# Performance work log

Hardware: AMD Instinct MI355X
Metric: run time of the kernel (lower is better)

## Reference

```python
import jax, jax.numpy as jnp
import numpy as np
import math

B, S, D, H = 2, 4096, 512, 8
DK = D // H


def setup_inputs() -> dict:
    key = jax.random.key(0)
    ks = jax.random.split(key, 9)
    s = 1.0 / math.sqrt(D)
    return {
        "x": jax.random.normal(ks[0], (B, S, D), dtype=jnp.float32),
        "Wq": jax.random.normal(ks[1], (D, D), dtype=jnp.float32) * s,
        "bq": jax.random.normal(ks[2], (D,), dtype=jnp.float32) * 0.01,
        "Wk": jax.random.normal(ks[3], (D, D), dtype=jnp.float32) * s,
        "bk": jax.random.normal(ks[4], (D,), dtype=jnp.float32) * 0.01,
        "Wv": jax.random.normal(ks[5], (D, D), dtype=jnp.float32) * s,
        "bv": jax.random.normal(ks[6], (D,), dtype=jnp.float32) * 0.01,
        "Wo": jax.random.normal(ks[7], (D, D), dtype=jnp.float32) * s,
        "bo": jax.random.normal(ks[8], (D,), dtype=jnp.float32) * 0.01,
    }


def reference(x, Wq, bq, Wk, bk, Wv, bv, Wo, bo):
    b, s, _ = x.shape
    # projections, split into heads: (b, h, s, dk)
    def proj(W, bias):
        return (x @ W.T + bias).reshape(b, s, H, DK).transpose(0, 2, 1, 3)
    Q, K, V = proj(Wq, bq), proj(Wk, bk), proj(Wv, bv)
    scale = 1.0 / math.sqrt(DK)
    scores = jnp.einsum("bhqd,bhkd->bhqk", Q, K) * scale  # (b,h,s,s)
    causal = jnp.tril(jnp.ones((s, s), dtype=bool))
    scores = jnp.where(causal[None, None], scores, -jnp.inf)
    attn = jax.nn.softmax(scores, axis=-1)
    out = jnp.einsum("bhqk,bhkd->bhqd", attn, V)
    out = out.transpose(0, 2, 1, 3).reshape(b, s, D)
    return out @ Wo.T + bo
```

## Files before the change

kernel.cpp:

```cpp
#include <hip/hip_runtime.h>
#include <hip/hip_bf16.h>

using u16    = unsigned short;
using u32    = unsigned int;
using bf16x8 = __attribute__((ext_vector_type(8))) __bf16;
using s16x4  = __attribute__((ext_vector_type(4))) short;
using f32x4  = __attribute__((ext_vector_type(4))) float;
using u16x4  = __attribute__((ext_vector_type(4))) unsigned short;
using u16x8  = __attribute__((ext_vector_type(8))) unsigned short;
using u32x2  = __attribute__((ext_vector_type(2))) unsigned int;
using u32x4  = __attribute__((ext_vector_type(4))) unsigned int;


static __device__ __forceinline__ u16 f2bf(float f) {
  unsigned int u = __float_as_uint(f);
  u += 0x7fffu + ((u >> 16) & 1u);
  return (u16)(u >> 16);
}
static __device__ __forceinline__ u32 pack2bf(float lo, float hi) {
  return __builtin_amdgcn_perm(__float_as_uint(hi), __float_as_uint(lo), 0x07060302u);
}

__global__ __launch_bounds__(256) void cvt_all(
    const float* __restrict__ x,  const float* __restrict__ wq,
    const float* __restrict__ wk, const float* __restrict__ wv,
    const float* __restrict__ wo,
    u16* __restrict__ xb, u16* __restrict__ wqb, u16* __restrict__ wkb,
    u16* __restrict__ wvb, u16* __restrict__ wob) {
  const int bx = blockIdx.x;
  const float* src;
  u16* dst;
  int i;
  if (bx < 4096) {
    src = x; dst = xb; i = bx * 256 + threadIdx.x;
  } else {
    const int t  = (bx - 4096) >> 8;
    const int lb = (bx - 4096) & 255;
    src = (t == 0) ? wq : (t == 1) ? wk : (t == 2) ? wv : wo;
    dst = (t == 0) ? wqb : (t == 1) ? wkb : (t == 2) ? wvb : wob;
    i = lb * 256 + threadIdx.x;
  }
  float4 v = reinterpret_cast<const float4*>(src)[i];
  u16x4 o = { f2bf(v.x), f2bf(v.y), f2bf(v.z), f2bf(v.w) };
  reinterpret_cast<u16x4*>(dst)[i] = o;
}

__global__ __launch_bounds__(256, 3) void gemm_qkv(const u16* __restrict__ A,
                                                   const u16* __restrict__ Wq,
                                                   const u16* __restrict__ Wk,
                                                   const u16* __restrict__ Wv,
                                                   const float* __restrict__ bqp,
                                                   const float* __restrict__ bkp,
                                                   const float* __restrict__ bvp,
                                                   u16* __restrict__ Qo,
                                                   u16* __restrict__ Ko,
                                                   u16* __restrict__ Vto) {
  const int which = blockIdx.z;
  const u16* W = (which == 0) ? Wq : (which == 1) ? Wk : Wv;
  const float* bias = (which == 0) ? bqp : (which == 1) ? bkp : bvp;

  __shared__ u16 sA[128 * 72];
  __shared__ u16 sB[128 * 72];
  const int row0 = blockIdx.x * 128;
  const int col0 = blockIdx.y * 128;
  const int tid  = threadIdx.x;
  const int lane = tid & 63;
  const int wave = tid >> 6;
  const int wm   = (wave & 1) * 64;
  const int wn   = (wave >> 1) * 64;
  const int ln   = lane & 15;
  const int quad = lane >> 4;

  int rr[4], cc[4];
  for (int i = 0; i < 4; ++i) {
    const int idx = tid + 256 * i;
    rr[i] = idx >> 3; cc[i] = (idx & 7) * 8;
  }

  f32x4 zero = {0.f, 0.f, 0.f, 0.f};
  f32x4 acc[4][4];
  for (int i = 0; i < 4; ++i)
    for (int j = 0; j < 4; ++j) acc[i][j] = zero;

  u16x8 curA[4], nxtA[4];
  for (int i = 0; i < 4; ++i)
    curA[i] = *reinterpret_cast<const u16x8*>(&A[(row0 + rr[i]) * 512 + cc[i]]);

  for (int k0 = 0; k0 < 512; k0 += 64) {
    __syncthreads();
    for (int i = 0; i < 4; ++i) {
      *reinterpret_cast<u16x8*>(&sA[rr[i] * 72 + cc[i]]) = curA[i];
      *reinterpret_cast<u16x8*>(&sB[rr[i] * 72 + cc[i]]) =
          *reinterpret_cast<const u16x8*>(&W[(col0 + rr[i]) * 512 + k0 + cc[i]]);
    }
    if (k0 < 448)
      for (int i = 0; i < 4; ++i)
        nxtA[i] = *reinterpret_cast<const u16x8*>(&A[(row0 + rr[i]) * 512 + k0 + 64 + cc[i]]);
    __syncthreads();
    for (int ks = 0; ks < 2; ++ks) {
      bf16x8 af[4], bfr[4];
      for (int t4 = 0; t4 < 4; ++t4)
        af[t4] = *reinterpret_cast<const bf16x8*>(&sA[(wm + t4 * 16 + ln) * 72 + ks * 32 + quad * 8]);
      for (int t4 = 0; t4 < 4; ++t4)
        bfr[t4] = *reinterpret_cast<const bf16x8*>(&sB[(wn + t4 * 16 + ln) * 72 + ks * 32 + quad * 8]);
      for (int tm = 0; tm < 4; ++tm)
        for (int tn = 0; tn < 4; ++tn)
          acc[tm][tn] = __builtin_amdgcn_mfma_f32_16x16x32_bf16(af[tm], bfr[tn], acc[tm][tn], 0, 0, 0);
    }
    for (int i = 0; i < 4; ++i) curA[i] = nxtA[i];
  }

  if (which < 2) {
    u16* out = (which == 0) ? Qo : Ko;
    const float scale = (which == 0) ? 0.125f : 1.0f;
    for (int tm = 0; tm < 4; ++tm) {
      const int mbase = row0 + wm + tm * 16 + quad * 4;
      for (int tn = 0; tn < 4; ++tn) {
        const int n  = col0 + wn + tn * 16 + ln;
        const int h  = n >> 6, dk = n & 63;
        const float bv = bias[n];
        for (int r = 0; r < 4; ++r) {
          const int m  = mbase + r;
          const int bh = ((m >> 12) << 3) + h;
          const int s  = m & 4095;
          out[(bh * 4096 + s) * 64 + dk] = f2bf((acc[tm][tn][r] + bv) * scale);
        }
      }
    }
  } else {
    for (int tm = 0; tm < 4; ++tm) {
      const int mbase = row0 + wm + tm * 16 + quad * 4;
      const int b_idx = mbase >> 12;
      const int s     = mbase & 4095;
      for (int tn = 0; tn < 4; ++tn) {
        const int n  = col0 + wn + tn * 16 + ln;
        const int h  = n >> 6, dk = n & 63;
        const int bh = b_idx * 8 + h;
        const float bv = bias[n];
        u16x4 o;
        for (int r = 0; r < 4; ++r) o[r] = f2bf(acc[tm][tn][r] + bv);
        *reinterpret_cast<u16x4*>(&Vto[(bh * 64 + dk) * 4096 + s]) = o;
      }
    }
  }
}

__global__ __launch_bounds__(256, 3) void gemm_out(const u16* __restrict__ A,
                                                   const u16* __restrict__ W,
                                                   const float* __restrict__ bias,
                                                   float* __restrict__ out) {
  __shared__ u16 sA[128 * 72];
  __shared__ u16 sB[128 * 72];
  const int row0 = blockIdx.x * 128;
  const int col0 = blockIdx.y * 128;
  const int tid  = threadIdx.x;
  const int lane = tid & 63;
  const int wave = tid >> 6;
  const int wm   = (wave & 1) * 64;
  const int wn   = (wave >> 1) * 64;
  const int ln   = lane & 15;
  const int quad = lane >> 4;

  int rr[4], cc[4];
  for (int i = 0; i < 4; ++i) {
    const int idx = tid + 256 * i;
    rr[i] = idx >> 3; cc[i] = (idx & 7) * 8;
  }

  f32x4 zero = {0.f, 0.f, 0.f, 0.f};
  f32x4 acc[4][4];
  for (int i = 0; i < 4; ++i)
    for (int j = 0; j < 4; ++j) acc[i][j] = zero;

  u16x8 curA[4], nxtA[4];
  for (int i = 0; i < 4; ++i)
    curA[i] = *reinterpret_cast<const u16x8*>(&A[(row0 + rr[i]) * 512 + cc[i]]);

  for (int k0 = 0; k0 < 512; k0 += 64) {
    __syncthreads();
    for (int i = 0; i < 4; ++i) {
      *reinterpret_cast<u16x8*>(&sA[rr[i] * 72 + cc[i]]) = curA[i];
      *reinterpret_cast<u16x8*>(&sB[rr[i] * 72 + cc[i]]) =
          *reinterpret_cast<const u16x8*>(&W[(col0 + rr[i]) * 512 + k0 + cc[i]]);
    }
    if (k0 < 448)
      for (int i = 0; i < 4; ++i)
        nxtA[i] = *reinterpret_cast<const u16x8*>(&A[(row0 + rr[i]) * 512 + k0 + 64 + cc[i]]);
    __syncthreads();
    for (int ks = 0; ks < 2; ++ks) {
      bf16x8 af[4], bfr[4];
      for (int t4 = 0; t4 < 4; ++t4)
        af[t4] = *reinterpret_cast<const bf16x8*>(&sA[(wm + t4 * 16 + ln) * 72 + ks * 32 + quad * 8]);
      for (int t4 = 0; t4 < 4; ++t4)
        bfr[t4] = *reinterpret_cast<const bf16x8*>(&sB[(wn + t4 * 16 + ln) * 72 + ks * 32 + quad * 8]);
      for (int tm = 0; tm < 4; ++tm)
        for (int tn = 0; tn < 4; ++tn)
          acc[tm][tn] = __builtin_amdgcn_mfma_f32_16x16x32_bf16(af[tm], bfr[tn], acc[tm][tn], 0, 0, 0);
    }
    for (int i = 0; i < 4; ++i) curA[i] = nxtA[i];
  }

  for (int tm = 0; tm < 4; ++tm) {
    const int mbase = row0 + wm + tm * 16 + quad * 4;
    for (int tn = 0; tn < 4; ++tn) {
      const int n  = col0 + wn + tn * 16 + ln;
      const float bv = bias[n];
      for (int r = 0; r < 4; ++r)
        out[(mbase + r) * 512 + n] = acc[tm][tn][r] + bv;
    }
  }
}

#if __has_builtin(__builtin_amdgcn_mfma_f32_16x16x16bf16_1k)
#define HAVE_MFMA16 1
#endif
__global__ __launch_bounds__(256, 4) void attn_part(const u16* __restrict__ Q,
                                                    const u16* __restrict__ K,
                                                    const u16* __restrict__ Vt,
                                                    float* __restrict__ pO,
                                                    float* __restrict__ pl) {
  const int c = blockIdx.x;
  const int t = blockIdx.y;
  const int ga = t >> 3;
  if (c > ga) return;
  const int ktlast = 2 * t + 1;
  const int kt0 = 16 * c;
  const int kt1 = (kt0 + 15 < ktlast) ? (kt0 + 15) : ktlast;
  const int bh = blockIdx.z;
  const int qb = t * 128;

  const u16* Qh  = Q  + bh * 4096 * 64;
  const u16* Kh  = K  + bh * 4096 * 64;
  const u16* Vth = Vt + bh * 64 * 4096;

  __shared__ u16 sK[64 * 72];
  __shared__ u16 sV[64 * 72];

  const int tid  = threadIdx.x;
  const int lane = tid & 63;
  const int wave = tid >> 6;
  const int ln   = lane & 15;
  const int quad = lane >> 4;

  const int r0 = tid >> 3,         c0 = (tid & 7) * 8;
  const int r1 = (tid + 256) >> 3, c1 = ((tid + 256) & 7) * 8;

  bf16x8 qf[2][2];
  for (int tn = 0; tn < 2; ++tn)
    for (int ks = 0; ks < 2; ++ks)
      qf[tn][ks] = *reinterpret_cast<const bf16x8*>(
          &Qh[(qb + wave * 32 + tn * 16 + ln) * 64 + ks * 32 + quad * 8]);

  f32x4 zero = {0.f, 0.f, 0.f, 0.f};
  f32x4 accO[4][2];
  float lsum[2] = {0.f, 0.f};
  for (int td = 0; td < 4; ++td)
    for (int tn = 0; tn < 2; ++tn) accO[td][tn] = zero;

#ifndef HAVE_MFMA16
  const int idx0 = 4 * (ln + 16 * (2 * (quad & 1)));
#endif

  u16x8 cur[4], nxt[4];
  {
    const int kb = kt0 * 64;
    cur[0] = *reinterpret_cast<const u16x8*>(&Kh[(kb + r0) * 64 + c0]);
    cur[1] = *reinterpret_cast<const u16x8*>(&Kh[(kb + r1) * 64 + c1]);
    cur[2] = *reinterpret_cast<const u16x8*>(&Vth[r0 * 4096 + kb + c0]);
    cur[3] = *reinterpret_cast<const u16x8*>(&Vth[r1 * 4096 + kb + c1]);
  }

  for (int kt = kt0; kt <= kt1; ++kt) {
    const int kb = kt * 64;
    __syncthreads();
    *reinterpret_cast<u16x8*>(&sK[r0 * 72 + c0]) = cur[0];
    *reinterpret_cast<u16x8*>(&sK[r1 * 72 + c1]) = cur[1];
    *reinterpret_cast<u16x8*>(&sV[r0 * 72 + c0]) = cur[2];
    *reinterpret_cast<u16x8*>(&sV[r1 * 72 + c1]) = cur[3];
    if (kt < kt1) {
      const int kn = kb + 64;
      nxt[0] = *reinterpret_cast<const u16x8*>(&Kh[(kn + r0) * 64 + c0]);
      nxt[1] = *reinterpret_cast<const u16x8*>(&Kh[(kn + r1) * 64 + c1]);
      nxt[2] = *reinterpret_cast<const u16x8*>(&Vth[r0 * 4096 + kn + c0]);
      nxt[3] = *reinterpret_cast<const u16x8*>(&Vth[r1 * 4096 + kn + c1]);
    }
    __syncthreads();

    f32x4 accS[4][2];
    for (int tm = 0; tm < 4; ++tm)
      for (int tn = 0; tn < 2; ++tn) accS[tm][tn] = zero;
    for (int tm = 0; tm < 4; ++tm) {
      bf16x8 kf0 = *reinterpret_cast<const bf16x8*>(&sK[(tm * 16 + ln) * 72 + quad * 8]);
      bf16x8 kf1 = *reinterpret_cast<const bf16x8*>(&sK[(tm * 16 + ln) * 72 + 32 + quad * 8]);
      for (int tn = 0; tn < 2; ++tn) {
        accS[tm][tn] = __builtin_amdgcn_mfma_f32_16x16x32_bf16(kf0, qf[tn][0], accS[tm][tn], 0, 0, 0);
        accS[tm][tn] = __builtin_amdgcn_mfma_f32_16x16x32_bf16(kf1, qf[tn][1], accS[tm][tn], 0, 0, 0);
      }
    }

    const bool diag = (kt >= 2 * t);
    u32 pp[4][2][2];
    for (int tm = 0; tm < 4; ++tm)
      for (int tn = 0; tn < 2; ++tn) {
        f32x4 e = accS[tm][tn];
        if (diag) {
          const int kg = kb + tm * 16 + quad * 4;
          const int qg = qb + wave * 32 + tn * 16 + ln;
          for (int r = 0; r < 4; ++r)
            if (kg + r > qg) e[r] = -__builtin_inff();
        }
        for (int r = 0; r < 4; ++r) e[r] = __expf(e[r]);
        lsum[tn] += (e[0] + e[1]) + (e[2] + e[3]);
        pp[tm][tn][0] = pack2bf(e[0], e[1]);
        pp[tm][tn][1] = pack2bf(e[2], e[3]);
      }

#ifdef HAVE_MFMA16
    for (int k16 = 0; k16 < 4; ++k16)
      for (int td = 0; td < 4; ++td) {
        s16x4 vf = *reinterpret_cast<const s16x4*>(&sV[(td * 16 + ln) * 72 + k16 * 16 + quad * 4]);
        for (int tn = 0; tn < 2; ++tn) {
          u32x2 pr = { pp[k16][tn][0], pp[k16][tn][1] };
          s16x4 pb = __builtin_bit_cast(s16x4, pr);
          accO[td][tn] = __builtin_amdgcn_mfma_f32_16x16x16bf16_1k(vf, pb, accO[td][tn], 0, 0, 0);
        }
      }
#else
    for (int ks = 0; ks < 2; ++ks)
      for (int tn = 0; tn < 2; ++tn) {
        u32 b[4];
        for (int half = 0; half < 2; ++half)
          for (int p = 0; p < 2; ++p) {
            int v0 = __builtin_amdgcn_ds_bpermute(idx0 + 64 * half, (int)pp[2 * ks][tn][p]);
            int v1 = __builtin_amdgcn_ds_bpermute(idx0 + 64 * half, (int)pp[2 * ks + 1][tn][p]);
            b[half * 2 + p] = (quad < 2) ? (u32)v0 : (u32)v1;
          }
        u32x4 bv4 = { b[0], b[1], b[2], b[3] };
        bf16x8 pfrag = __builtin_bit_cast(bf16x8, bv4);
        for (int td = 0; td < 4; ++td) {
          bf16x8 vf = *reinterpret_cast<const bf16x8*>(&sV[(td * 16 + ln) * 72 + ks * 32 + quad * 8]);
          accO[td][tn] = __builtin_amdgcn_mfma_f32_16x16x32_bf16(vf, pfrag, accO[td][tn], 0, 0, 0);
        }
      }
#endif
    for (int j = 0; j < 4; ++j) cur[j] = nxt[j];
  }

  for (int tn = 0; tn < 2; ++tn) {
    lsum[tn] += __shfl_xor(lsum[tn], 16);
    lsum[tn] += __shfl_xor(lsum[tn], 32);
  }
  const int slot = bh * 80 + t + 4 * ga * (ga - 1) + ga * (t & 7) + c;
  float* po = pO + (size_t)slot * 8192;
  for (int td = 0; td < 4; ++td)
    for (int tn = 0; tn < 2; ++tn)
      for (int r = 0; r < 4; ++r)
        po[(td * 16 + quad * 4 + r) * 128 + wave * 32 + tn * 16 + ln] = accO[td][tn][r];
  if (quad == 0)
    for (int tn = 0; tn < 2; ++tn)
      pl[slot * 128 + wave * 32 + tn * 16 + ln] = lsum[tn];
}

__global__ __launch_bounds__(256) void attn_comb(const float* __restrict__ pO,
                                                 const float* __restrict__ pl,
                                                 u16* __restrict__ ctx) {
  const int t  = blockIdx.x;
  const int bh = blockIdx.y;
  const int ga = t >> 3;
  const int nch = ga + 1;
  const int base = bh * 80 + t + 4 * ga * (ga - 1) + ga * (t & 7);
  const int tid = threadIdx.x;

  __shared__ float sO[64 * 132];
  __shared__ float sL[128];

  float4 acc[8];
  for (int i = 0; i < 8; ++i) acc[i] = make_float4(0.f, 0.f, 0.f, 0.f);
  float lacc = 0.f;
  for (int cidx = 0; cidx < nch; ++cidx) {
    const float* src = pO + (size_t)(base + cidx) * 8192;
    for (int i = 0; i < 8; ++i) {
      float4 v = reinterpret_cast<const float4*>(src)[i * 256 + tid];
      acc[i].x += v.x; acc[i].y += v.y; acc[i].z += v.z; acc[i].w += v.w;
    }
    if (tid < 128) lacc += pl[(base + cidx) * 128 + tid];
  }
  for (int i = 0; i < 8; ++i) {
    const int f = i * 256 + tid;
    const int d = f >> 5, q = (f & 31) * 4;
    *reinterpret_cast<float4*>(&sO[d * 132 + q]) = acc[i];
  }
  if (tid < 128) sL[tid] = lacc;
  __syncthreads();

  const int q  = tid >> 1;
  const int d0 = (tid & 1) * 32;
  const float inv = 1.0f / sL[q];
  const int b_idx = bh >> 3, h = bh & 7;
  const int tok = (b_idx << 12) + t * 128 + q;
  u16* dst = &ctx[tok * 512 + h * 64 + d0];
  for (int g = 0; g < 4; ++g) {
    u16x8 ov;
    for (int j = 0; j < 8; ++j) ov[j] = f2bf(sO[(d0 + g * 8 + j) * 132 + q] * inv);
    *reinterpret_cast<u16x8*>(&dst[g * 8]) = ov;
  }
}

extern "C" void kernel_launch(void* const* d_in, const int* in_sizes, int n_in,
                              void* d_out, int out_size, void* d_ws, size_t ws_size,
                              hipStream_t stream) {
  const float* x  = (const float*)d_in[0];
  const float* Wq = (const float*)d_in[1];
  const float* bq = (const float*)d_in[2];
  const float* Wk = (const float*)d_in[3];
  const float* bk = (const float*)d_in[4];
  const float* Wv = (const float*)d_in[5];
  const float* bv = (const float*)d_in[6];
  const float* Wo = (const float*)d_in[7];
  const float* bo = (const float*)d_in[8];
  float* out = (float*)d_out;

  char* ws = (char*)d_ws;
  u16* xb  = (u16*)(ws + 0);
  u16* wqb = (u16*)(ws + 8388608);
  u16* wkb = (u16*)(ws + 8912896);
  u16* wvb = (u16*)(ws + 9437184);
  u16* wob = (u16*)(ws + 9961472);
  u16* Qb  = (u16*)(ws + 10485760);
  u16* Kb  = (u16*)(ws + 18874368);
  u16* Vtb = (u16*)(ws + 27262976);
  float* pO = (float*)(ws + 35651584);
  float* pl = (float*)(ws + 77594624);
  u16* ctx = xb;

  cvt_all<<<5120, 256, 0, stream>>>(x, Wq, Wk, Wv, Wo, xb, wqb, wkb, wvb, wob);
  gemm_qkv<<<dim3(64, 4, 3), 256, 0, stream>>>(xb, wqb, wkb, wvb, bq, bk, bv, Qb, Kb, Vtb);
  attn_part<<<dim3(4, 32, 16), 256, 0, stream>>>(Qb, Kb, Vtb, pO, pl);
  attn_comb<<<dim3(32, 16), 256, 0, stream>>>(pO, pl, ctx);
  gemm_out<<<dim3(64, 4), 256, 0, stream>>>(ctx, wob, bo, out);
}
```

Before: 205.2 us.

## Split attention into finer KV chunks, double-buffer K/V LDS, shrink output GEMM tile

Attention partial kernel now splits each query tile's KV range into chunks of 8 tiles instead of 16, doubling the split-K parallelism and changing the slot layout and combine indexing to match. K/V shared memory is double-buffered so the next tile's stores overlap with compute, dropping one barrier per iteration. The output GEMM uses 64-row tiles with more blocks and higher occupancy. The costs are more partial-output traffic and more combine work, plus a larger workspace footprint.

```diff
diff --git a/kernel.cpp b/kernel.cpp
--- a/kernel.cpp
+++ b/kernel.cpp
@@ -145,18 +145,18 @@
   }
 }
 
-__global__ __launch_bounds__(256, 3) void gemm_out(const u16* __restrict__ A,
+__global__ __launch_bounds__(256, 4) void gemm_out(const u16* __restrict__ A,
                                                    const u16* __restrict__ W,
                                                    const float* __restrict__ bias,
                                                    float* __restrict__ out) {
-  __shared__ u16 sA[128 * 72];
+  __shared__ u16 sA[64 * 72];
   __shared__ u16 sB[128 * 72];
-  const int row0 = blockIdx.x * 128;
+  const int row0 = blockIdx.x * 64;
   const int col0 = blockIdx.y * 128;
   const int tid  = threadIdx.x;
   const int lane = tid & 63;
   const int wave = tid >> 6;
-  const int wm   = (wave & 1) * 64;
+  const int wm   = (wave & 1) * 32;
   const int wn   = (wave >> 1) * 64;
   const int ln   = lane & 15;
   const int quad = lane >> 4;
@@ -168,39 +168,39 @@
   }
 
   f32x4 zero = {0.f, 0.f, 0.f, 0.f};
-  f32x4 acc[4][4];
-  for (int i = 0; i < 4; ++i)
+  f32x4 acc[2][4];
+  for (int i = 0; i < 2; ++i)
     for (int j = 0; j < 4; ++j) acc[i][j] = zero;
 
-  u16x8 curA[4], nxtA[4];
-  for (int i = 0; i < 4; ++i)
+  u16x8 curA[2], nxtA[2];
+  for (int i = 0; i < 2; ++i)
     curA[i] = *reinterpret_cast<const u16x8*>(&A[(row0 + rr[i]) * 512 + cc[i]]);
 
   for (int k0 = 0; k0 < 512; k0 += 64) {
     __syncthreads();
-    for (int i = 0; i < 4; ++i) {
+    for (int i = 0; i < 2; ++i)
       *reinterpret_cast<u16x8*>(&sA[rr[i] * 72 + cc[i]]) = curA[i];
+    for (int i = 0; i < 4; ++i)
       *reinterpret_cast<u16x8*>(&sB[rr[i] * 72 + cc[i]]) =
           *reinterpret_cast<const u16x8*>(&W[(col0 + rr[i]) * 512 + k0 + cc[i]]);
-    }
     if (k0 < 448)
-      for (int i = 0; i < 4; ++i)
+      for (int i = 0; i < 2; ++i)
         nxtA[i] = *reinterpret_cast<const u16x8*>(&A[(row0 + rr[i]) * 512 + k0 + 64 + cc[i]]);
     __syncthreads();
     for (int ks = 0; ks < 2; ++ks) {
-      bf16x8 af[4], bfr[4];
-      for (int t4 = 0; t4 < 4; ++t4)
+      bf16x8 af[2], bfr[4];
+      for (int t4 = 0; t4 < 2; ++t4)
         af[t4] = *reinterpret_cast<const bf16x8*>(&sA[(wm + t4 * 16 + ln) * 72 + ks * 32 + quad * 8]);
       for (int t4 = 0; t4 < 4; ++t4)
         bfr[t4] = *reinterpret_cast<const bf16x8*>(&sB[(wn + t4 * 16 + ln) * 72 + ks * 32 + quad * 8]);
-      for (int tm = 0; tm < 4; ++tm)
+      for (int tm = 0; tm < 2; ++tm)
         for (int tn = 0; tn < 4; ++tn)
           acc[tm][tn] = __builtin_amdgcn_mfma_f32_16x16x32_bf16(af[tm], bfr[tn], acc[tm][tn], 0, 0, 0);
     }
-    for (int i = 0; i < 4; ++i) curA[i] = nxtA[i];
-  }
-
-  for (int tm = 0; tm < 4; ++tm) {
+    for (int i = 0; i < 2; ++i) curA[i] = nxtA[i];
+  }
+
+  for (int tm = 0; tm < 2; ++tm) {
     const int mbase = row0 + wm + tm * 16 + quad * 4;
     for (int tn = 0; tn < 4; ++tn) {
       const int n  = col0 + wn + tn * 16 + ln;
@@ -221,11 +221,11 @@
                                                     float* __restrict__ pl) {
   const int c = blockIdx.x;
   const int t = blockIdx.y;
-  const int ga = t >> 3;
-  if (c > ga) return;
+  const int g = t >> 2;
+  if (c > g) return;
   const int ktlast = 2 * t + 1;
-  const int kt0 = 16 * c;
-  const int kt1 = (kt0 + 15 < ktlast) ? (kt0 + 15) : ktlast;
+  const int kt0 = 8 * c;
+  const int kt1 = (kt0 + 7 < ktlast) ? (kt0 + 7) : ktlast;
   const int bh = blockIdx.z;
   const int qb = t * 128;
 
@@ -233,8 +233,8 @@
   const u16* Kh  = K  + bh * 4096 * 64;
   const u16* Vth = Vt + bh * 64 * 4096;
 
-  __shared__ u16 sK[64 * 72];
-  __shared__ u16 sV[64 * 72];
+  __shared__ u16 sK[2][64 * 72];
+  __shared__ u16 sV[2][64 * 72];
 
   const int tid  = threadIdx.x;
   const int lane = tid & 63;
@@ -268,30 +268,45 @@
     cur[1] = *reinterpret_cast<const u16x8*>(&Kh[(kb + r1) * 64 + c1]);
     cur[2] = *reinterpret_cast<const u16x8*>(&Vth[r0 * 4096 + kb + c0]);
     cur[3] = *reinterpret_cast<const u16x8*>(&Vth[r1 * 4096 + kb + c1]);
-  }
-
+    *reinterpret_cast<u16x8*>(&sK[0][r0 * 72 + c0]) = cur[0];
+    *reinterpret_cast<u16x8*>(&sK[0][r1 * 72 + c1]) = cur[1];
+    *reinterpret_cast<u16x8*>(&sV[0][r0 * 72 + c0]) = cur[2];
+    *reinterpret_cast<u16x8*>(&sV[0][r1 * 72 + c1]) = cur[3];
+    const int kn = kb + 64;
+    cur[0] = *reinterpret_cast<const u16x8*>(&Kh[(kn + r0) * 64 + c0]);
+    cur[1] = *reinterpret_cast<const u16x8*>(&Kh[(kn + r1) * 64 + c1]);
+    cur[2] = *reinterpret_cast<const u16x8*>(&Vth[r0 * 4096 + kn + c0]);
+    cur[3] = *reinterpret_cast<const u16x8*>(&Vth[r1 * 4096 + kn + c1]);
+  }
+
+  int pb = 0;
   for (int kt = kt0; kt <= kt1; ++kt) {
     const int kb = kt * 64;
     __syncthreads();
-    *reinterpret_cast<u16x8*>(&sK[r0 * 72 + c0]) = cur[0];
-    *reinterpret_cast<u16x8*>(&sK[r1 * 72 + c1]) = cur[1];
-    *reinterpret_cast<u16x8*>(&sV[r0 * 72 + c0]) = cur[2];
-    *reinterpret_cast<u16x8*>(&sV[r1 * 72 + c1]) = cur[3];
     if (kt < kt1) {
-      const int kn = kb + 64;
-      nxt[0] = *reinterpret_cast<const u16x8*>(&Kh[(kn + r0) * 64 + c0]);
-      nxt[1] = *reinterpret_cast<const u16x8*>(&Kh[(kn + r1) * 64 + c1]);
-      nxt[2] = *reinterpret_cast<const u16x8*>(&Vth[r0 * 4096 + kn + c0]);
-      nxt[3] = *reinterpret_cast<const u16x8*>(&Vth[r1 * 4096 + kn + c1]);
-    }
-    __syncthreads();
+      u16* dK = sK[pb ^ 1];
+      u16* dV = sV[pb ^ 1];
+      *reinterpret_cast<u16x8*>(&dK[r0 * 72 + c0]) = cur[0];
+      *reinterpret_cast<u16x8*>(&dK[r1 * 72 + c1]) = cur[1];
+      *reinterpret_cast<u16x8*>(&dV[r0 * 72 + c0]) = cur[2];
+      *reinterpret_cast<u16x8*>(&dV[r1 * 72 + c1]) = cur[3];
+      if (kt + 2 <= kt1) {
+        const int kn = kb + 128;
+        nxt[0] = *reinterpret_cast<const u16x8*>(&Kh[(kn + r0) * 64 + c0]);
+        nxt[1] = *reinterpret_cast<const u16x8*>(&Kh[(kn + r1) * 64 + c1]);
+        nxt[2] = *reinterpret_cast<const u16x8*>(&Vth[r0 * 4096 + kn + c0]);
+        nxt[3] = *reinterpret_cast<const u16x8*>(&Vth[r1 * 4096 + kn + c1]);
+      }
+    }
+    const u16* bK = sK[pb];
+    const u16* bV = sV[pb];
 
     f32x4 accS[4][2];
     for (int tm = 0; tm < 4; ++tm)
       for (int tn = 0; tn < 2; ++tn) accS[tm][tn] = zero;
     for (int tm = 0; tm < 4; ++tm) {
-      bf16x8 kf0 = *reinterpret_cast<const bf16x8*>(&sK[(tm * 16 + ln) * 72 + quad * 8]);
-      bf16x8 kf1 = *reinterpret_cast<const bf16x8*>(&sK[(tm * 16 + ln) * 72 + 32 + quad * 8]);
+      bf16x8 kf0 = *reinterpret_cast<const bf16x8*>(&bK[(tm * 16 + ln) * 72 + quad * 8]);
+      bf16x8 kf1 = *reinterpret_cast<const bf16x8*>(&bK[(tm * 16 + ln) * 72 + 32 + quad * 8]);
       for (int tn = 0; tn < 2; ++tn) {
         accS[tm][tn] = __builtin_amdgcn_mfma_f32_16x16x32_bf16(kf0, qf[tn][0], accS[tm][tn], 0, 0, 0);
         accS[tm][tn] = __builtin_amdgcn_mfma_f32_16x16x32_bf16(kf1, qf[tn][1], accS[tm][tn], 0, 0, 0);
@@ -318,11 +333,11 @@
 #ifdef HAVE_MFMA16
     for (int k16 = 0; k16 < 4; ++k16)
       for (int td = 0; td < 4; ++td) {
-        s16x4 vf = *reinterpret_cast<const s16x4*>(&sV[(td * 16 + ln) * 72 + k16 * 16 + quad * 4]);
+        s16x4 vf = *reinterpret_cast<const s16x4*>(&bV[(td * 16 + ln) * 72 + k16 * 16 + quad * 4]);
         for (int tn = 0; tn < 2; ++tn) {
           u32x2 pr = { pp[k16][tn][0], pp[k16][tn][1] };
-          s16x4 pb = __builtin_bit_cast(s16x4, pr);
-          accO[td][tn] = __builtin_amdgcn_mfma_f32_16x16x16bf16_1k(vf, pb, accO[td][tn], 0, 0, 0);
+          s16x4 pbv = __builtin_bit_cast(s16x4, pr);
+          accO[td][tn] = __builtin_amdgcn_mfma_f32_16x16x16bf16_1k(vf, pbv, accO[td][tn], 0, 0, 0);
         }
       }
 #else
@@ -338,19 +353,20 @@
         u32x4 bv4 = { b[0], b[1], b[2], b[3] };
         bf16x8 pfrag = __builtin_bit_cast(bf16x8, bv4);
         for (int td = 0; td < 4; ++td) {
-          bf16x8 vf = *reinterpret_cast<const bf16x8*>(&sV[(td * 16 + ln) * 72 + ks * 32 + quad * 8]);
+          bf16x8 vf = *reinterpret_cast<const bf16x8*>(&bV[(td * 16 + ln) * 72 + ks * 32 + quad * 8]);
           accO[td][tn] = __builtin_amdgcn_mfma_f32_16x16x32_bf16(vf, pfrag, accO[td][tn], 0, 0, 0);
         }
       }
 #endif
     for (int j = 0; j < 4; ++j) cur[j] = nxt[j];
+    pb ^= 1;
   }
 
   for (int tn = 0; tn < 2; ++tn) {
     lsum[tn] += __shfl_xor(lsum[tn], 16);
     lsum[tn] += __shfl_xor(lsum[tn], 32);
   }
-  const int slot = bh * 80 + t + 4 * ga * (ga - 1) + ga * (t & 7) + c;
+  const int slot = bh * 144 + t + 2 * g * (g - 1) + (t & 3) * g + c;
   float* po = pO + (size_t)slot * 8192;
   for (int td = 0; td < 4; ++td)
     for (int tn = 0; tn < 2; ++tn)
@@ -366,9 +382,9 @@
                                                  u16* __restrict__ ctx) {
   const int t  = blockIdx.x;
   const int bh = blockIdx.y;
-  const int ga = t >> 3;
-  const int nch = ga + 1;
-  const int base = bh * 80 + t + 4 * ga * (ga - 1) + ga * (t & 7);
+  const int g  = t >> 2;
+  const int nch = g + 1;
+  const int base = bh * 144 + t + 2 * g * (g - 1) + (t & 3) * g;
   const int tid = threadIdx.x;
 
   __shared__ float sO[64 * 132];
@@ -399,10 +415,10 @@
   const int b_idx = bh >> 3, h = bh & 7;
   const int tok = (b_idx << 12) + t * 128 + q;
   u16* dst = &ctx[tok * 512 + h * 64 + d0];
-  for (int g = 0; g < 4; ++g) {
+  for (int gI = 0; gI < 4; ++gI) {
     u16x8 ov;
-    for (int j = 0; j < 8; ++j) ov[j] = f2bf(sO[(d0 + g * 8 + j) * 132 + q] * inv);
-    *reinterpret_cast<u16x8*>(&dst[g * 8]) = ov;
+    for (int j = 0; j < 8; ++j) ov[j] = f2bf(sO[(d0 + gI * 8 + j) * 132 + q] * inv);
+    *reinterpret_cast<u16x8*>(&dst[gI * 8]) = ov;
   }
 }
 
@@ -430,12 +446,12 @@
   u16* Kb  = (u16*)(ws + 18874368);
   u16* Vtb = (u16*)(ws + 27262976);
   float* pO = (float*)(ws + 35651584);
-  float* pl = (float*)(ws + 77594624);
+  float* pl = (float*)(ws + 111149056);
   u16* ctx = xb;
 
   cvt_all<<<5120, 256, 0, stream>>>(x, Wq, Wk, Wv, Wo, xb, wqb, wkb, wvb, wob);
   gemm_qkv<<<dim3(64, 4, 3), 256, 0, stream>>>(xb, wqb, wkb, wvb, bq, bk, bv, Qb, Kb, Vtb);
-  attn_part<<<dim3(4, 32, 16), 256, 0, stream>>>(Qb, Kb, Vtb, pO, pl);
+  attn_part<<<dim3(8, 32, 16), 256, 0, stream>>>(Qb, Kb, Vtb, pO, pl);
   attn_comb<<<dim3(32, 16), 256, 0, stream>>>(pO, pl, ctx);
-  gemm_out<<<dim3(64, 4), 256, 0, stream>>>(ctx, wob, bo, out);
-}
+  gemm_out<<<dim3(128, 4), 256, 0, stream>>>(ctx, wob, bo, out);
+}
```

Result: slower. 209.7 us (+2.2%).
